# Performance work log

Measured on AMD Instinct MI355X. Metric: run time of the kernel, lower is better.

The kernel has to match this reference:

```python
import jax, jax.numpy as jnp
import numpy as np

B, S, H, DH = 2, 2048, 16, 64
D = H * DH          # 1024, model width = num_heads * m_dim
OUT = 1024
NEG = -1e9


def setup_inputs() -> dict:
    key = jax.random.key(0)
    ks = jax.random.split(key, 10)
    x = jax.random.normal(ks[0], (B, S, D), dtype=jnp.float32)
    # padding mask [B, S, 1] of 0/1 floats
    mask = jax.random.randint(ks[1], (B, S, 1), 0, 2).astype(jnp.float32)
    def lin(k, din, dout):
        # xavier_uniform-ish init for weights stored as [din, dout]
        lim = float(np.sqrt(6.0 / (din + dout)))
        return jax.random.uniform(k, (din, dout), jnp.float32, -lim, lim)
    return {
        "x": x, "mask": mask,
        "Wq": lin(ks[2], D, D), "bq": jnp.zeros((D,), jnp.float32),
        "Wk": lin(ks[3], D, D), "bk": jnp.zeros((D,), jnp.float32),
        "Wv": lin(ks[4], D, D), "bv": jnp.zeros((D,), jnp.float32),
        "Wo": lin(ks[5], D, OUT), "bo": jnp.zeros((OUT,), jnp.float32),
    }


def reference(x, mask, Wq, bq, Wk, bk, Wv, bv, Wo, bo):
    # mask: [B,S,1] -> pairwise mask [B,S,S]
    mask_att = mask * jnp.swapaxes(mask, -1, -2)          # [B,S,S]
    q = (x @ Wq + bq).reshape(B, S, H, DH)
    k = (x @ Wk + bk).reshape(B, S, H, DH)
    v = (x @ Wv + bv).reshape(B, S, H, DH)
    # scores: [B,H,S,S]; multiplicative mask applied BEFORE scaling (as in source)
    scores = jnp.einsum('bqhd,bkhd->bhqk', q, k) * mask_att[:, None]
    scores = scores / jnp.sqrt(jnp.float32(DH))
    scores = scores + (1.0 - mask_att[:, None]) * NEG
    w = jax.nn.softmax(scores, axis=-1) * mask_att[:, None]
    msgs = jnp.einsum('bhqk,bkhd->bqhd', w, v).reshape(B, S, D)
    return msgs @ Wo + bo
```

## Files before the change

kernel.cpp:

```cpp
#include <hip/hip_runtime.h>
#include <hip/hip_bf16.h>
#include <math.h>

#define B_   2
#define S_   2048
#define H_   16
#define DH_  64
#define D_   1024
#define OUT_ 1024
#define M_   (B_ * S_)

typedef __attribute__((ext_vector_type(8))) short bf16x8;
typedef __attribute__((ext_vector_type(4))) float f32x4;
typedef __attribute__((ext_vector_type(4))) short short4v;

#define MFMA(a, b, c) __builtin_amdgcn_mfma_f32_16x16x32_bf16((a), (b), (c), 0, 0, 0)

__device__ __forceinline__ void gl_lds16(const void* g, void* l) {
    __builtin_amdgcn_global_load_lds(
        (const __attribute__((address_space(1))) unsigned int*)g,
        (__attribute__((address_space(3))) unsigned int*)l, 16, 0, 0);
}

__device__ __forceinline__ void split2(float x, unsigned short& h, unsigned short& l) {
    unsigned u = __float_as_uint(x);
    h = (unsigned short)(u >> 16);
    float lo = x - __uint_as_float(u & 0xFFFF0000u);
    l = (unsigned short)(__float_as_uint(lo) >> 16);
}

__device__ __forceinline__ unsigned short bf16_rne(float x) {
    return __builtin_bit_cast(unsigned short, __float2bfloat16(x));
}

__device__ __forceinline__ float fast_exp2(float x) {
#if __has_builtin(__builtin_amdgcn_exp2f)
    return __builtin_amdgcn_exp2f(x);
#else
    return exp2f(x);
#endif
}

__global__ __launch_bounds__(256)
void scan_mask(const float* __restrict__ mask, int* __restrict__ cpos,
               int* __restrict__ opos, int* __restrict__ nv)
{
    __shared__ int cnt[256];
    const int b = blockIdx.x, tid = threadIdx.x;
    const int base = b * 2048 + tid * 8;
    int mloc = 0, c = 0;
    #pragma unroll
    for (int i = 0; i < 8; ++i) {
        const int v = (mask[base + i] != 0.f) ? 1 : 0;
        mloc |= v << i;
        c += v;
    }
    cnt[tid] = c;
    __syncthreads();
    for (int off = 1; off < 256; off <<= 1) {
        const int v = cnt[tid];
        const int add = (tid >= off) ? cnt[tid - off] : 0;
        __syncthreads();
        cnt[tid] = v + add;
        __syncthreads();
    }
    int excl = cnt[tid] - c;
    #pragma unroll
    for (int i = 0; i < 8; ++i) {
        cpos[base + i] = excl;
        if ((mloc >> i) & 1) {
            opos[b * 2048 + excl] = tid * 8 + i;
            ++excl;
        }
    }
    if (tid == 255) nv[b] = cnt[255];
}

__global__ __launch_bounds__(256)
void split_x_c(const float* __restrict__ X, const float* __restrict__ mask,
               const int* __restrict__ cpos,
               unsigned short* __restrict__ Xh, unsigned short* __restrict__ Xl)
{
    const int row = blockIdx.x;
    const int b = row >> 11, s = row & 2047;
    if (mask[(size_t)b * 2048 + s] == 0.f) return;
    const int cr = b * 2048 + cpos[b * 2048 + s];
    const int c4 = threadIdx.x * 4;
    const float4 v = *(const float4*)&X[(size_t)row * D_ + c4];
    unsigned short h[4], l[4];
    split2(v.x, h[0], l[0]); split2(v.y, h[1], l[1]);
    split2(v.z, h[2], l[2]); split2(v.w, h[3], l[3]);
    *(short4v*)&Xh[(size_t)cr * D_ + c4] =
        (short4v){(short)h[0],(short)h[1],(short)h[2],(short)h[3]};
    *(short4v*)&Xl[(size_t)cr * D_ + c4] =
        (short4v){(short)l[0],(short)l[1],(short)l[2],(short)l[3]};
}

__global__ __launch_bounds__(256)
void fill_out(float* __restrict__ out, const float* __restrict__ bo)
{
    const int i = blockIdx.x * 256 + threadIdx.x;
    ((float4*)out)[i] = ((const float4*)bo)[i & 255];
}

__global__ __launch_bounds__(256)
void tconv_w(const float* __restrict__ W, unsigned short* __restrict__ Th,
             unsigned short* __restrict__ Tl, int K, int N)
{
    __shared__ float T[64][65];
    const int tid = threadIdx.x;
    const int k0 = blockIdx.x * 64, n0 = blockIdx.y * 64;
    #pragma unroll
    for (int p = 0; p < 4; ++p) {
        const int f = p * 256 + tid;
        const int r = f >> 4, c4 = (f & 15) << 2;
        const float4 v = *(const float4*)&W[(size_t)(k0 + r) * N + n0 + c4];
        T[r][c4] = v.x; T[r][c4 + 1] = v.y; T[r][c4 + 2] = v.z; T[r][c4 + 3] = v.w;
    }
    __syncthreads();
    #pragma unroll
    for (int p = 0; p < 4; ++p) {
        const int f = p * 256 + tid;
        const int r = f >> 4, c4 = (f & 15) << 2;
        unsigned short h[4], l[4];
        #pragma unroll
        for (int i = 0; i < 4; ++i) split2(T[c4 + i][r], h[i], l[i]);
        *(short4v*)&Th[(size_t)(n0 + r) * K + k0 + c4] =
            (short4v){(short)h[0],(short)h[1],(short)h[2],(short)h[3]};
        *(short4v*)&Tl[(size_t)(n0 + r) * K + k0 + c4] =
            (short4v){(short)l[0],(short)l[1],(short)l[2],(short)l[3]};
    }
}

__global__ __launch_bounds__(256)
void tconv_qkv(const float* __restrict__ W0, const float* __restrict__ W1,
               const float* __restrict__ W2, unsigned short* __restrict__ Th,
               unsigned short* __restrict__ Tl)
{
    __shared__ float T[64][65];
    const int z = blockIdx.z;
    const float* W = (z == 0) ? W0 : (z == 1) ? W1 : W2;
    unsigned short* th = Th + ((size_t)z << 20);
    unsigned short* tl = Tl + ((size_t)z << 20);
    const int tid = threadIdx.x;
    const int k0 = blockIdx.x * 64, n0 = blockIdx.y * 64;
    #pragma unroll
    for (int p = 0; p < 4; ++p) {
        const int f = p * 256 + tid;
        const int r = f >> 4, c4 = (f & 15) << 2;
        const float4 v = *(const float4*)&W[(size_t)(k0 + r) * D_ + n0 + c4];
        T[r][c4] = v.x; T[r][c4 + 1] = v.y; T[r][c4 + 2] = v.z; T[r][c4 + 3] = v.w;
    }
    __syncthreads();
    #pragma unroll
    for (int p = 0; p < 4; ++p) {
        const int f = p * 256 + tid;
        const int r = f >> 4, c4 = (f & 15) << 2;
        unsigned short h[4], l[4];
        #pragma unroll
        for (int i = 0; i < 4; ++i) split2(T[c4 + i][r], h[i], l[i]);
        *(short4v*)&th[(size_t)(n0 + r) * D_ + k0 + c4] =
            (short4v){(short)h[0],(short)h[1],(short)h[2],(short)h[3]};
        *(short4v*)&tl[(size_t)(n0 + r) * D_ + k0 + c4] =
            (short4v){(short)l[0],(short)l[1],(short)l[2],(short)l[3]};
    }
}

__global__ __launch_bounds__(256, 3)
void gemm_qkv(const unsigned short* __restrict__ Ah, const unsigned short* __restrict__ Al,
              const unsigned short* __restrict__ Bh, const unsigned short* __restrict__ Bl,
              const float* __restrict__ bq, const float* __restrict__ bk,
              const float* __restrict__ bv,
              unsigned short* __restrict__ Oqh, unsigned short* __restrict__ Oql,
              unsigned short* __restrict__ Okh, unsigned short* __restrict__ Ovt,
              const int* __restrict__ nv)
{
    const int n0 = blockIdx.x * 64, m0 = blockIdx.y * 128;
    const int bb = m0 >> 11;
    const int nvb = nv[bb];
    if ((m0 & 2047) >= nvb) return;

    __shared__ unsigned short As_h[128 * 64], As_l[128 * 64];
    __shared__ unsigned short Bs_h[64 * 64],  Bs_l[64 * 64];

    const int tid = threadIdx.x;
    const int lane = tid & 63, w = tid >> 6;
    const int wm = w >> 1, wn = w & 1;
    const int l15 = lane & 15, l4 = lane >> 4;
    const int lr = lane >> 3, lc = lane & 7;
    const int idx = n0 >> 10;

    f32x4 acc[4][2];
    #pragma unroll
    for (int i = 0; i < 4; ++i)
        #pragma unroll
        for (int j = 0; j < 2; ++j) acc[i][j] = (f32x4){0.f, 0.f, 0.f, 0.f};

    for (int kt = 0; kt < D_; kt += 64) {
        __syncthreads();
        #pragma unroll
        for (int t = 0; t < 4; ++t) {
            const int row = w * 32 + t * 8 + lr;
            const int kc = lc ^ (row & 7);
            const size_t g = (size_t)(m0 + row) * D_ + kt + kc * 8;
            gl_lds16(&Ah[g], &As_h[(w * 32 + t * 8) * 64]);
            if (idx == 0)
                gl_lds16(&Al[g], &As_l[(w * 32 + t * 8) * 64]);
        }
        #pragma unroll
        for (int t = 0; t < 2; ++t) {
            const int row = w * 16 + t * 8 + lr;
            const int kc = lc ^ (row & 7);
            const size_t g = (size_t)(n0 + row) * D_ + kt + kc * 8;
            gl_lds16(&Bh[g], &Bs_h[(w * 16 + t * 8) * 64]);
            gl_lds16(&Bl[g], &Bs_l[(w * 16 + t * 8) * 64]);
        }
        __syncthreads();

        #pragma unroll
        for (int kk = 0; kk < 2; ++kk) {
            bf16x8 ah[4], bh2[2], bl2[2];
            #pragma unroll
            for (int i = 0; i < 4; ++i) {
                const int row = wm * 64 + i * 16 + l15;
                const int off = row * 64 + (((kk * 4 + l4) ^ (row & 7)) << 3);
                ah[i] = *(const bf16x8*)&As_h[off];
            }
            #pragma unroll
            for (int j = 0; j < 2; ++j) {
                const int row = wn * 32 + j * 16 + l15;
                const int off = row * 64 + (((kk * 4 + l4) ^ (row & 7)) << 3);
                bh2[j] = *(const bf16x8*)&Bs_h[off];
                bl2[j] = *(const bf16x8*)&Bs_l[off];
            }
            #pragma unroll
            for (int i = 0; i < 4; ++i)
                #pragma unroll
                for (int j = 0; j < 2; ++j) {
                    acc[i][j] = MFMA(ah[i], bh2[j], acc[i][j]);
                    acc[i][j] = MFMA(ah[i], bl2[j], acc[i][j]);
                }
            if (idx == 0) {
                #pragma unroll
                for (int i = 0; i < 4; ++i) {
                    const int row = wm * 64 + i * 16 + l15;
                    const int off = row * 64 + (((kk * 4 + l4) ^ (row & 7)) << 3);
                    const bf16x8 al = *(const bf16x8*)&As_l[off];
                    #pragma unroll
                    for (int j = 0; j < 2; ++j)
                        acc[i][j] = MFMA(al, bh2[j], acc[i][j]);
                }
            }
        }
    }

    const float* bp = (idx == 0) ? bq : (idx == 1) ? bk : bv;
    #pragma unroll
    for (int i = 0; i < 4; ++i) {
        const int m = m0 + wm * 64 + i * 16 + l4 * 4;
        const int jm = m & 2047;
        #pragma unroll
        for (int j = 0; j < 2; ++j) {
            const int nG = n0 + wn * 32 + j * 16 + l15;
            const int c = nG & 1023;
            const float bvv = bp[c];
            const int hh = c >> 6, dd = c & 63;
            if (idx == 0) {
                const size_t base = ((size_t)(bb * H_ + hh) * S_ + jm) * 64 + dd;
                #pragma unroll
                for (int r = 0; r < 4; ++r)
                    if (jm + r < nvb) {
                        unsigned short vh, vl;
                        split2(acc[i][j][r] + bvv, vh, vl);
                        Oqh[base + (size_t)r * 64] = vh;
                        Oql[base + (size_t)r * 64] = vl;
                    }
            } else if (idx == 1) {
                const size_t base = ((size_t)(bb * H_ + hh) * S_ + jm) * 64 + dd;
                #pragma unroll
                for (int r = 0; r < 4; ++r)
                    if (jm + r < nvb)
                        Okh[base + (size_t)r * 64] = bf16_rne(acc[i][j][r] + bvv);
            } else {
                unsigned short pv[4];
                #pragma unroll
                for (int r = 0; r < 4; ++r) pv[r] = bf16_rne(acc[i][j][r] + bvv);
                const size_t vb = ((size_t)(bb * H_ + hh) * 64 + dd) * (size_t)S_ + jm;
                if (jm + 3 < nvb) {
                    *(short4v*)&Ovt[vb] =
                        (short4v){(short)pv[0],(short)pv[1],(short)pv[2],(short)pv[3]};
                } else {
                    #pragma unroll
                    for (int r = 0; r < 4; ++r)
                        if (jm + r < nvb) Ovt[vb + r] = pv[r];
                }
            }
        }
    }
}

__global__ __launch_bounds__(256, 4)
void gemm_out64(const unsigned short* __restrict__ Ah, const unsigned short* __restrict__ Al,
                const unsigned short* __restrict__ Bh, const unsigned short* __restrict__ Bl,
                const float* __restrict__ bias, float* __restrict__ Cf,
                const int* __restrict__ nv, const int* __restrict__ opos)
{
    const int n0 = blockIdx.x * 64, m0 = blockIdx.y * 64;
    const int bb = m0 >> 11;
    const int nvb = nv[bb];
    if ((m0 & 2047) >= nvb) return;

    __shared__ unsigned short As_h[64 * 64], As_l[64 * 64];
    __shared__ unsigned short Bs_h[64 * 64], Bs_l[64 * 64];

    const int tid = threadIdx.x;
    const int lane = tid & 63, w = tid >> 6;
    const int wm = w >> 1, wn = w & 1;
    const int l15 = lane & 15, l4 = lane >> 4;
    const int lr = lane >> 3, lc = lane & 7;

    f32x4 acc[2][2];
    #pragma unroll
    for (int i = 0; i < 2; ++i)
        #pragma unroll
        for (int j = 0; j < 2; ++j) acc[i][j] = (f32x4){0.f, 0.f, 0.f, 0.f};

    for (int kt = 0; kt < D_; kt += 64) {
        __syncthreads();
        #pragma unroll
        for (int t = 0; t < 2; ++t) {
            const int row = w * 16 + t * 8 + lr;
            const int kc = lc ^ (row & 7);
            const size_t ga = (size_t)(m0 + row) * D_ + kt + kc * 8;
            gl_lds16(&Ah[ga], &As_h[(w * 16 + t * 8) * 64]);
            gl_lds16(&Al[ga], &As_l[(w * 16 + t * 8) * 64]);
            const size_t gb = (size_t)(n0 + row) * D_ + kt + kc * 8;
            gl_lds16(&Bh[gb], &Bs_h[(w * 16 + t * 8) * 64]);
            gl_lds16(&Bl[gb], &Bs_l[(w * 16 + t * 8) * 64]);
        }
        __syncthreads();

        #pragma unroll
        for (int kk = 0; kk < 2; ++kk) {
            bf16x8 ah[2], al[2], bh2[2], bl2[2];
            #pragma unroll
            for (int i = 0; i < 2; ++i) {
                const int row = wm * 32 + i * 16 + l15;
                const int off = row * 64 + (((kk * 4 + l4) ^ (row & 7)) << 3);
                ah[i] = *(const bf16x8*)&As_h[off];
                al[i] = *(const bf16x8*)&As_l[off];
            }
            #pragma unroll
            for (int j = 0; j < 2; ++j) {
                const int row = wn * 32 + j * 16 + l15;
                const int off = row * 64 + (((kk * 4 + l4) ^ (row & 7)) << 3);
                bh2[j] = *(const bf16x8*)&Bs_h[off];
                bl2[j] = *(const bf16x8*)&Bs_l[off];
            }
            #pragma unroll
            for (int i = 0; i < 2; ++i)
                #pragma unroll
                for (int j = 0; j < 2; ++j) {
                    acc[i][j] = MFMA(ah[i], bh2[j], acc[i][j]);
                    acc[i][j] = MFMA(ah[i], bl2[j], acc[i][j]);
                    acc[i][j] = MFMA(al[i], bh2[j], acc[i][j]);
                }
        }
    }

    const int* op = opos + bb * 2048;
    #pragma unroll
    for (int i = 0; i < 2; ++i) {
        const int m = m0 + wm * 32 + i * 16 + l4 * 4;
        #pragma unroll
        for (int j = 0; j < 2; ++j) {
            const int n = n0 + wn * 32 + j * 16 + l15;
            const float bvv = bias[n];
            #pragma unroll
            for (int r = 0; r < 4; ++r) {
                const int jr = (m & 2047) + r;
                if (jr < nvb)
                    Cf[((size_t)bb * 2048 + op[jr]) * OUT_ + n] = acc[i][j][r] + bvv;
            }
        }
    }
}

__global__ __launch_bounds__(512, 4)
void attn_mfma(const unsigned short* __restrict__ Qh, const unsigned short* __restrict__ Ql,
               const unsigned short* __restrict__ Kh, const unsigned short* __restrict__ Vt,
               const int* __restrict__ nv,
               unsigned short* __restrict__ Mh, unsigned short* __restrict__ Ml)
{
    const int bh = blockIdx.x, b = bh >> 4;
    const int nvb = nv[b];
    const int q0 = blockIdx.y * 128;
    if (q0 >= nvb) return;

    __shared__ unsigned short Ks[2][64 * 64];
    __shared__ unsigned short Vts[2][64 * 64];
    __shared__ unsigned short Psb[128 * 72];

    const float SC2  = 0.125f * 1.4426950408889634f;
    const float THR2 = 11.5415603f;
    const float MINIT = -1e5f;
    const float NEGB  = -1e30f;

    const int tid = threadIdx.x;
    const int lane = tid & 63, w = tid >> 6;
    const int l15 = lane & 15, l4 = lane >> 4;
    const int qw = q0 + w * 16;

    const int srow = w * 8 + (lane >> 3);
    const int skc  = (lane & 7) ^ (srow & 7);

    bf16x8 qh[2], ql[2];
    {
        const int qr = min(qw + l15, nvb - 1);
        const size_t qbase = ((size_t)bh * S_ + qr) * 64;
        #pragma unroll
        for (int kk = 0; kk < 2; ++kk) {
            qh[kk] = *(const bf16x8*)&Qh[qbase + kk * 32 + l4 * 8];
            ql[kk] = *(const bf16x8*)&Ql[qbase + kk * 32 + l4 * 8];
        }
    }

    float m2[4], lp[4];
    f32x4 O[4];
    #pragma unroll
    for (int r = 0; r < 4; ++r) { m2[r] = MINIT; lp[r] = 0.f; }
    #pragma unroll
    for (int df = 0; df < 4; ++df) O[df] = (f32x4){0.f, 0.f, 0.f, 0.f};

    const int NT = (nvb + 63) >> 6;

#define STAGE(KT, SEL)                                                          \
    do {                                                                        \
        gl_lds16(&Kh[((size_t)bh * S_ + (KT) + srow) * 64 + skc * 8],           \
                 &Ks[SEL][(w * 8) * 64]);                                       \
        gl_lds16(&Vt[((size_t)bh * 64 + srow) * (size_t)S_ + (KT) + skc * 8],   \
                 &Vts[SEL][(w * 8) * 64]);                                      \
    } while (0)

    STAGE(0, 0);
    __syncthreads();

    int cur = 0;
    for (int ti = 0; ti < NT; ++ti, cur ^= 1) {
        const int kt = ti * 64;
        if (ti + 1 < NT) STAGE((ti + 1) * 64, cur ^ 1);

        f32x4 s[4];
        #pragma unroll
        for (int nf = 0; nf < 4; ++nf) s[nf] = (f32x4){0.f, 0.f, 0.f, 0.f};
        #pragma unroll
        for (int nf = 0; nf < 4; ++nf) {
            const int krow = nf * 16 + l15;
            #pragma unroll
            for (int kk = 0; kk < 2; ++kk) {
                const int off = krow * 64 + (((kk * 4 + l4) ^ (krow & 7)) << 3);
                const bf16x8 kh8 = *(const bf16x8*)&Ks[cur][off];
                s[nf] = MFMA(qh[kk], kh8, s[nf]);
                s[nf] = MFMA(ql[kk], kh8, s[nf]);
            }
        }

        float addk[4];
        #pragma unroll
        for (int nf = 0; nf < 4; ++nf)
            addk[nf] = (kt + nf * 16 + l15 < nvb) ? 0.f : NEGB;

        float lm[4];
        bool need = false;
        #pragma unroll
        for (int r = 0; r < 4; ++r) {
            float v0 = fmaf(s[0][r], SC2, addk[0]);
            float v1 = fmaf(s[1][r], SC2, addk[1]);
            float v2 = fmaf(s[2][r], SC2, addk[2]);
            float v3 = fmaf(s[3][r], SC2, addk[3]);
            s[0][r] = v0; s[1][r] = v1; s[2][r] = v2; s[3][r] = v3;
            const float rm = fmaxf(fmaxf(v0, v1), fmaxf(v2, v3));
            lm[r] = rm;
            need |= (rm > m2[r] + THR2);
        }

        if (__any(need)) {
            #pragma unroll
            for (int r = 0; r < 4; ++r) {
                float rm = lm[r];
                rm = fmaxf(rm, __shfl_xor(rm, 1));
                rm = fmaxf(rm, __shfl_xor(rm, 2));
                rm = fmaxf(rm, __shfl_xor(rm, 4));
                rm = fmaxf(rm, __shfl_xor(rm, 8));
                const float mnew = fmaxf(m2[r], rm);
                const float sc = fast_exp2(m2[r] - mnew);
                lp[r] *= sc;
                m2[r] = mnew;
                #pragma unroll
                for (int df = 0; df < 4; ++df) O[df][r] *= sc;
            }
        }

        #pragma unroll
        for (int r = 0; r < 4; ++r) {
            const float mm = m2[r];
            const int qq = w * 16 + l4 * 4 + r;
            const int qbase = qq * 72;
            const int qswz = qq & 7;
            float rs = 0.f;
            #pragma unroll
            for (int nf = 0; nf < 4; ++nf) {
                const float pv = fast_exp2(s[nf][r] - mm);
                rs += pv;
                const int key = nf * 16 + l15;
                Psb[qbase + (((key >> 3) ^ qswz) << 3) + (key & 7)] = bf16_rne(pv);
            }
            lp[r] += rs;
        }

        #pragma unroll
        for (int kk = 0; kk < 2; ++kk) {
            const int qq = w * 16 + l15;
            const bf16x8 ph = *(const bf16x8*)
                &Psb[qq * 72 + ((((kk * 4) + l4) ^ (qq & 7)) << 3)];
            #pragma unroll
            for (int df = 0; df < 4; ++df) {
                const int vrow = df * 16 + l15;
                const int off = vrow * 64 + (((kk * 4 + l4) ^ (vrow & 7)) << 3);
                const bf16x8 vb = *(const bf16x8*)&Vts[cur][off];
                O[df] = MFMA(ph, vb, O[df]);
            }
        }

        __syncthreads();
    }
#undef STAGE

    #pragma unroll
    for (int r = 0; r < 4; ++r) {
        float t = lp[r];
        t += __shfl_xor(t, 1);
        t += __shfl_xor(t, 2);
        t += __shfl_xor(t, 4);
        t += __shfl_xor(t, 8);
        const int j = qw + l4 * 4 + r;
        if (j < nvb) {
            const float inv = (t > 0.f) ? 1.f / t : 0.f;
            const size_t base = ((size_t)b * S_ + j) * D_ + (bh & 15) * DH_;
            #pragma unroll
            for (int df = 0; df < 4; ++df) {
                unsigned short vh, vl;
                split2(O[df][r] * inv, vh, vl);
                Mh[base + df * 16 + l15] = vh;
                Ml[base + df * 16 + l15] = vl;
            }
        }
    }
}

extern "C" void kernel_launch(void* const* d_in, const int* in_sizes, int n_in,
                              void* d_out, int out_size, void* d_ws, size_t ws_size,
                              hipStream_t stream)
{
    const float* x    = (const float*)d_in[0];
    const float* mask = (const float*)d_in[1];
    const float* Wq   = (const float*)d_in[2];
    const float* bq   = (const float*)d_in[3];
    const float* Wk   = (const float*)d_in[4];
    const float* bk   = (const float*)d_in[5];
    const float* Wv   = (const float*)d_in[6];
    const float* bv   = (const float*)d_in[7];
    const float* Wo   = (const float*)d_in[8];
    const float* bo   = (const float*)d_in[9];
    float* out = (float*)d_out;

    char* ws = (char*)d_ws;
    unsigned short* xh = (unsigned short*)(ws);
    unsigned short* xl = (unsigned short*)(ws + ((size_t) 8 << 20));
    unsigned short* qh = (unsigned short*)(ws + ((size_t)16 << 20));
    unsigned short* qll= (unsigned short*)(ws + ((size_t)24 << 20));
    unsigned short* kh = (unsigned short*)(ws + ((size_t)32 << 20));
    unsigned short* vt = (unsigned short*)(ws + ((size_t)40 << 20));
    unsigned short* wc_h = (unsigned short*)(ws + ((size_t)48 << 20));
    unsigned short* wc_l = (unsigned short*)(ws + ((size_t)54 << 20));
    unsigned short* wo_h = wc_h;
    unsigned short* wo_l = (unsigned short*)(ws + ((size_t)50 << 20));
    unsigned short* mh = xh;
    unsigned short* ml = xl;
    int* cpos = (int*)(ws + ((size_t)60 << 20));
    int* opos = (int*)(ws + ((size_t)60 << 20) + 16384);
    int* nv   = (int*)(ws + ((size_t)60 << 20) + 32768);

    const dim3 blk(256);
    scan_mask<<<dim3(B_), blk, 0, stream>>>(mask, cpos, opos, nv);
    split_x_c<<<dim3(M_), blk, 0, stream>>>(x, mask, cpos, xh, xl);
    tconv_qkv<<<dim3(16, 16, 3), blk, 0, stream>>>(Wq, Wk, Wv, wc_h, wc_l);

    gemm_qkv<<<dim3(3 * D_ / 64, M_ / 128), blk, 0, stream>>>(
        xh, xl, wc_h, wc_l, bq, bk, bv, qh, qll, kh, vt, nv);

    tconv_w<<<dim3(16, 16), blk, 0, stream>>>(Wo, wo_h, wo_l, D_, OUT_);

    attn_mfma<<<dim3(B_ * H_, S_ / 128), dim3(512), 0, stream>>>(
        qh, qll, kh, vt, nv, mh, ml);

    fill_out<<<dim3(M_ * OUT_ / 4 / 256), blk, 0, stream>>>(out, bo);

    gemm_out64<<<dim3(OUT_ / 64, M_ / 64), blk, 0, stream>>>(
        mh, ml, wo_h, wo_l, bo, out, nv, opos);
}
```

Baseline: 150.2 us.

## Double-buffer LDS tiles in QKV and output GEMMs with K-step of 32

Both split-bf16 GEMM kernels now keep two LDS buffers of 32-wide K slices. Each iteration issues the global-to-LDS loads for the next slice before computing on the current one, so memory latency overlaps with MFMA work. The XOR swizzle changes from 8-way to 4-way to match the narrower rows. The cost is twice as many loop iterations and barriers, each doing half the compute. The buffers stay the same total size, but the single barrier per step relies on the async LDS loads having completed.

```diff
diff --git a/kernel.cpp b/kernel.cpp
--- a/kernel.cpp
+++ b/kernel.cpp
@@ -180,14 +180,14 @@
     const int nvb = nv[bb];
     if ((m0 & 2047) >= nvb) return;
 
-    __shared__ unsigned short As_h[128 * 64], As_l[128 * 64];
-    __shared__ unsigned short Bs_h[64 * 64],  Bs_l[64 * 64];
+    __shared__ unsigned short As_h[2][128 * 32], As_l[2][128 * 32];
+    __shared__ unsigned short Bs_h[2][64 * 32],  Bs_l[2][64 * 32];
 
     const int tid = threadIdx.x;
     const int lane = tid & 63, w = tid >> 6;
     const int wm = w >> 1, wn = w & 1;
     const int l15 = lane & 15, l4 = lane >> 4;
-    const int lr = lane >> 3, lc = lane & 7;
+    const int srow4 = lane >> 2, sch = lane & 3;
     const int idx = n0 >> 10;
 
     f32x4 acc[4][2];
@@ -196,63 +196,68 @@
         #pragma unroll
         for (int j = 0; j < 2; ++j) acc[i][j] = (f32x4){0.f, 0.f, 0.f, 0.f};
 
-    for (int kt = 0; kt < D_; kt += 64) {
-        __syncthreads();
-        #pragma unroll
-        for (int t = 0; t < 4; ++t) {
-            const int row = w * 32 + t * 8 + lr;
-            const int kc = lc ^ (row & 7);
-            const size_t g = (size_t)(m0 + row) * D_ + kt + kc * 8;
-            gl_lds16(&Ah[g], &As_h[(w * 32 + t * 8) * 64]);
-            if (idx == 0)
-                gl_lds16(&Al[g], &As_l[(w * 32 + t * 8) * 64]);
-        }
-        #pragma unroll
-        for (int t = 0; t < 2; ++t) {
-            const int row = w * 16 + t * 8 + lr;
-            const int kc = lc ^ (row & 7);
-            const size_t g = (size_t)(n0 + row) * D_ + kt + kc * 8;
-            gl_lds16(&Bh[g], &Bs_h[(w * 16 + t * 8) * 64]);
-            gl_lds16(&Bl[g], &Bs_l[(w * 16 + t * 8) * 64]);
-        }
-        __syncthreads();
-
-        #pragma unroll
-        for (int kk = 0; kk < 2; ++kk) {
-            bf16x8 ah[4], bh2[2], bl2[2];
+#define QKV_STAGE(KT, SEL)                                                      \
+    do {                                                                        \
+        _Pragma("unroll")                                                       \
+        for (int t = 0; t < 2; ++t) {               \
+            const int ar = w * 32 + t * 16 + srow4;                             \
+            const int kc = sch ^ (ar & 3);                                      \
+            const size_t g = (size_t)(m0 + ar) * D_ + (KT) + kc * 8;            \
+            gl_lds16(&Ah[g], &As_h[SEL][(w * 32 + t * 16) * 32]);               \
+            if (idx == 0)                                                       \
+                gl_lds16(&Al[g], &As_l[SEL][(w * 32 + t * 16) * 32]);           \
+        }                                                                       \
+        {                                           \
+            const int br = w * 16 + srow4;                                      \
+            const int kc = sch ^ (br & 3);                                      \
+            const size_t g = (size_t)(n0 + br) * D_ + (KT) + kc * 8;            \
+            gl_lds16(&Bh[g], &Bs_h[SEL][(w * 16) * 32]);                        \
+            gl_lds16(&Bl[g], &Bs_l[SEL][(w * 16) * 32]);                        \
+        }                                                                       \
+    } while (0)
+
+    QKV_STAGE(0, 0);
+    __syncthreads();
+
+    int cur = 0;
+    for (int kt = 0; kt < D_; kt += 32, cur ^= 1) {
+        if (kt + 32 < D_) QKV_STAGE(kt + 32, cur ^ 1);
+
+        bf16x8 ah[4], bh2[2], bl2[2];
+        #pragma unroll
+        for (int i = 0; i < 4; ++i) {
+            const int row = wm * 64 + i * 16 + l15;
+            ah[i] = *(const bf16x8*)&As_h[cur][row * 32 + ((l4 ^ (row & 3)) << 3)];
+        }
+        #pragma unroll
+        for (int j = 0; j < 2; ++j) {
+            const int row = wn * 32 + j * 16 + l15;
+            const int off = row * 32 + ((l4 ^ (row & 3)) << 3);
+            bh2[j] = *(const bf16x8*)&Bs_h[cur][off];
+            bl2[j] = *(const bf16x8*)&Bs_l[cur][off];
+        }
+        #pragma unroll
+        for (int i = 0; i < 4; ++i)
+            #pragma unroll
+            for (int j = 0; j < 2; ++j) {
+                acc[i][j] = MFMA(ah[i], bh2[j], acc[i][j]);
+                acc[i][j] = MFMA(ah[i], bl2[j], acc[i][j]);
+            }
+        if (idx == 0) {
             #pragma unroll
             for (int i = 0; i < 4; ++i) {
                 const int row = wm * 64 + i * 16 + l15;
-                const int off = row * 64 + (((kk * 4 + l4) ^ (row & 7)) << 3);
-                ah[i] = *(const bf16x8*)&As_h[off];
-            }
-            #pragma unroll
-            for (int j = 0; j < 2; ++j) {
-                const int row = wn * 32 + j * 16 + l15;
-                const int off = row * 64 + (((kk * 4 + l4) ^ (row & 7)) << 3);
-                bh2[j] = *(const bf16x8*)&Bs_h[off];
-                bl2[j] = *(const bf16x8*)&Bs_l[off];
-            }
-            #pragma unroll
-            for (int i = 0; i < 4; ++i)
+                const bf16x8 al = *(const bf16x8*)
+                    &As_l[cur][row * 32 + ((l4 ^ (row & 3)) << 3)];
                 #pragma unroll
-                for (int j = 0; j < 2; ++j) {
-                    acc[i][j] = MFMA(ah[i], bh2[j], acc[i][j]);
-                    acc[i][j] = MFMA(ah[i], bl2[j], acc[i][j]);
-                }
-            if (idx == 0) {
-                #pragma unroll
-                for (int i = 0; i < 4; ++i) {
-                    const int row = wm * 64 + i * 16 + l15;
-                    const int off = row * 64 + (((kk * 4 + l4) ^ (row & 7)) << 3);
-                    const bf16x8 al = *(const bf16x8*)&As_l[off];
-                    #pragma unroll
-                    for (int j = 0; j < 2; ++j)
-                        acc[i][j] = MFMA(al, bh2[j], acc[i][j]);
-                }
-            }
-        }
-    }
+                for (int j = 0; j < 2; ++j)
+                    acc[i][j] = MFMA(al, bh2[j], acc[i][j]);
+            }
+        }
+
+        __syncthreads();
+    }
+#undef QKV_STAGE
 
     const float* bp = (idx == 0) ? bq : (idx == 1) ? bk : bv;
     #pragma unroll
@@ -310,14 +315,14 @@
     const int nvb = nv[bb];
     if ((m0 & 2047) >= nvb) return;
 
-    __shared__ unsigned short As_h[64 * 64], As_l[64 * 64];
-    __shared__ unsigned short Bs_h[64 * 64], Bs_l[64 * 64];
+    __shared__ unsigned short As_h[2][64 * 32], As_l[2][64 * 32];
+    __shared__ unsigned short Bs_h[2][64 * 32], Bs_l[2][64 * 32];
 
     const int tid = threadIdx.x;
     const int lane = tid & 63, w = tid >> 6;
     const int wm = w >> 1, wn = w & 1;
     const int l15 = lane & 15, l4 = lane >> 4;
-    const int lr = lane >> 3, lc = lane & 7;
+    const int srow4 = lane >> 2, sch = lane & 3;
 
     f32x4 acc[2][2];
     #pragma unroll
@@ -325,48 +330,52 @@
         #pragma unroll
         for (int j = 0; j < 2; ++j) acc[i][j] = (f32x4){0.f, 0.f, 0.f, 0.f};
 
-    for (int kt = 0; kt < D_; kt += 64) {
+#define OUT_STAGE(KT, SEL)                                                      \
+    do {                                                                        \
+        const int r1 = w * 16 + srow4;                                          \
+        const int kc = sch ^ (r1 & 3);                                          \
+        const size_t ga = (size_t)(m0 + r1) * D_ + (KT) + kc * 8;               \
+        gl_lds16(&Ah[ga], &As_h[SEL][(w * 16) * 32]);                           \
+        gl_lds16(&Al[ga], &As_l[SEL][(w * 16) * 32]);                           \
+        const size_t gb = (size_t)(n0 + r1) * D_ + (KT) + kc * 8;               \
+        gl_lds16(&Bh[gb], &Bs_h[SEL][(w * 16) * 32]);                           \
+        gl_lds16(&Bl[gb], &Bs_l[SEL][(w * 16) * 32]);                           \
+    } while (0)
+
+    OUT_STAGE(0, 0);
+    __syncthreads();
+
+    int cur = 0;
+    for (int kt = 0; kt < D_; kt += 32, cur ^= 1) {
+        if (kt + 32 < D_) OUT_STAGE(kt + 32, cur ^ 1);
+
+        bf16x8 ah[2], al[2], bh2[2], bl2[2];
+        #pragma unroll
+        for (int i = 0; i < 2; ++i) {
+            const int row = wm * 32 + i * 16 + l15;
+            const int off = row * 32 + ((l4 ^ (row & 3)) << 3);
+            ah[i] = *(const bf16x8*)&As_h[cur][off];
+            al[i] = *(const bf16x8*)&As_l[cur][off];
+        }
+        #pragma unroll
+        for (int j = 0; j < 2; ++j) {
+            const int row = wn * 32 + j * 16 + l15;
+            const int off = row * 32 + ((l4 ^ (row & 3)) << 3);
+            bh2[j] = *(const bf16x8*)&Bs_h[cur][off];
+            bl2[j] = *(const bf16x8*)&Bs_l[cur][off];
+        }
+        #pragma unroll
+        for (int i = 0; i < 2; ++i)
+            #pragma unroll
+            for (int j = 0; j < 2; ++j) {
+                acc[i][j] = MFMA(ah[i], bh2[j], acc[i][j]);
+                acc[i][j] = MFMA(ah[i], bl2[j], acc[i][j]);
+                acc[i][j] = MFMA(al[i], bh2[j], acc[i][j]);
+            }
+
         __syncthreads();
-        #pragma unroll
-        for (int t = 0; t < 2; ++t) {
-            const int row = w * 16 + t * 8 + lr;
-            const int kc = lc ^ (row & 7);
-            const size_t ga = (size_t)(m0 + row) * D_ + kt + kc * 8;
-            gl_lds16(&Ah[ga], &As_h[(w * 16 + t * 8) * 64]);
-            gl_lds16(&Al[ga], &As_l[(w * 16 + t * 8) * 64]);
-            const size_t gb = (size_t)(n0 + row) * D_ + kt + kc * 8;
-            gl_lds16(&Bh[gb], &Bs_h[(w * 16 + t * 8) * 64]);
-            gl_lds16(&Bl[gb], &Bs_l[(w * 16 + t * 8) * 64]);
-        }
-        __syncthreads();
-
-        #pragma unroll
-        for (int kk = 0; kk < 2; ++kk) {
-            bf16x8 ah[2], al[2], bh2[2], bl2[2];
-            #pragma unroll
-            for (int i = 0; i < 2; ++i) {
-                const int row = wm * 32 + i * 16 + l15;
-                const int off = row * 64 + (((kk * 4 + l4) ^ (row & 7)) << 3);
-                ah[i] = *(const bf16x8*)&As_h[off];
-                al[i] = *(const bf16x8*)&As_l[off];
-            }
-            #pragma unroll
-            for (int j = 0; j < 2; ++j) {
-                const int row = wn * 32 + j * 16 + l15;
-                const int off = row * 64 + (((kk * 4 + l4) ^ (row & 7)) << 3);
-                bh2[j] = *(const bf16x8*)&Bs_h[off];
-                bl2[j] = *(const bf16x8*)&Bs_l[off];
-            }
-            #pragma unroll
-            for (int i = 0; i < 2; ++i)
-                #pragma unroll
-                for (int j = 0; j < 2; ++j) {
-                    acc[i][j] = MFMA(ah[i], bh2[j], acc[i][j]);
-                    acc[i][j] = MFMA(ah[i], bl2[j], acc[i][j]);
-                    acc[i][j] = MFMA(al[i], bh2[j], acc[i][j]);
-                }
-        }
-    }
+    }
+#undef OUT_STAGE
 
     const int* op = opos + bb * 2048;
     #pragma unroll
```

Result: slower. 167.8 us (+11.7%).
